# Kernel tuning notes

Measured on AMD Instinct MI355X. Metric: run time of the kernel, lower is better.

## Reference

```python
import jax, jax.numpy as jnp
import numpy as np

R = 4          # self.radius
NS = 256       # self.out_num_samples


def conv2d(x, w, b=None, padding=1, dilation=1):
    out = jax.lax.conv_general_dilated(
        x, w, window_strides=(1, 1),
        padding=[(padding, padding), (padding, padding)],
        rhs_dilation=(dilation, dilation),
        dimension_numbers=('NCHW', 'OIHW', 'NCHW'))
    if b is not None:
        out = out + b[None, :, None, None]
    return out


def depth_regression(logits):
    # softmax over 256 depth hypotheses, then expectation over a 9-wide
    # window centered at the argmax (clamped to [0, NS-1]).
    prob = jax.nn.softmax(logits, axis=1)                      # [B,256,H,W]
    amax = jnp.argmax(prob, axis=1, keepdims=True)             # [B,1,H,W] int
    offs = jnp.arange(-R, R + 1).reshape(1, 2 * R + 1, 1, 1)
    idx = jnp.clip(amax + offs, 0, NS - 1)                     # [B,9,H,W]
    p = jnp.take_along_axis(prob, idx, axis=1)                 # [B,9,H,W]
    num = jnp.sum(idx.astype(prob.dtype) * p, axis=1, keepdims=True)
    den = 1e-6 + jnp.sum(p, axis=1, keepdims=True)
    nd = (num / den) / (NS - 1.0)                              # [B,1,H,W]
    return nd, prob


def setup_inputs() -> dict:
    key = jax.random.key(0)
    ks = jax.random.split(key, 16)
    B, H, W = 4, 256, 320
    HD = 32            # hidden_dim
    CD = 32            # corr channels; input_dim = CD + 1 = 33
    CIN = HD + 1 + CD  # 65, GRU conv input channels

    def w(k, shape):
        fan = int(np.prod(shape[1:]))
        return (jax.random.normal(k, shape, jnp.float32) / np.sqrt(fan)).astype(jnp.float32)

    return {
        'hidden': jnp.tanh(jax.random.normal(ks[0], (B, HD, H, W), jnp.float32)),
        'normalized_depth': jax.random.uniform(ks[1], (B, 1, H, W), dtype=jnp.float32),
        'corr': jax.random.normal(ks[2], (B, CD, H, W), jnp.float32),
        # ConvGRU params (3x3, padding 1, with bias)
        'convz_w': w(ks[3], (HD, CIN, 3, 3)), 'convz_b': jnp.zeros((HD,), jnp.float32),
        'convr_w': w(ks[4], (HD, CIN, 3, 3)), 'convr_b': jnp.zeros((HD,), jnp.float32),
        'convq_w': w(ks[5], (HD, CIN, 3, 3)), 'convq_b': jnp.zeros((HD,), jnp.float32),
        # depth_head: 3x3 dil2 (no bias) -> 1x1 (no bias) -> 1x1 (bias)
        'dh1_w': w(ks[6], (32, HD, 3, 3)),
        'dh2_w': w(ks[7], (64, 32, 1, 1)),
        'dh3_w': w(ks[8], (NS, 64, 1, 1)), 'dh3_b': jnp.zeros((NS,), jnp.float32),
        # confidence_head: 3x3 dil2 (no bias) -> 1x1 (bias)
        'ch1_w': w(ks[9], (32, HD, 3, 3)),
        'ch2_w': w(ks[10], (1, 32, 1, 1)), 'ch2_b': jnp.zeros((1,), jnp.float32),
    }


def reference(hidden, normalized_depth, corr,
              convz_w, convz_b, convr_w, convr_b, convq_w, convq_b,
              dh1_w, dh2_w, dh3_w, dh3_b, ch1_w, ch2_w, ch2_b):
    # cat = [normalized_depth, corr]
    x = jnp.concatenate([normalized_depth, corr], axis=1)      # [B,33,H,W]
    # ConvGRU (confidence=None branch)
    hx = jnp.concatenate([hidden, x], axis=1)                  # [B,65,H,W]
    z = jax.nn.sigmoid(conv2d(hx, convz_w, convz_b))
    r = jax.nn.sigmoid(conv2d(hx, convr_w, convr_b))
    q = jnp.tanh(conv2d(jnp.concatenate([r * hidden, x], axis=1), convq_w, convq_b))
    h = (1.0 - z) * hidden + z * q                             # [B,32,H,W]
    # confidence head (confidence_flag=True)
    conf0 = conv2d(jax.nn.relu(conv2d(h, ch1_w, padding=2, dilation=2)),
                   ch2_w, ch2_b, padding=0)                    # [B,1,H,W]
    conf = jax.nn.sigmoid(conf0)
    # depth head
    t = jax.nn.relu(conv2d(h, dh1_w, padding=2, dilation=2))
    t = jax.nn.relu(conv2d(t, dh2_w, padding=0))
    logits = conv2d(t, dh3_w, dh3_b, padding=0)                # [B,256,H,W]
    nd, prob = depth_regression(logits)
    return h, nd, prob, conf, conf0
```

## Files before the change

### kernel.cpp

```cpp
#include <hip/hip_runtime.h>

#define WDT 320
#define HGT 256
#define HWSZ 81920
#define NPIX 327680

__device__ __forceinline__ float sigm(float x){ return 1.0f/(1.0f + __expf(-x)); }
__device__ __forceinline__ float tanh_(float x){
  float e = __expf(-2.0f*fabsf(x));
  float t = (1.0f - e)/(1.0f + e);
  return x < 0.0f ? -t : t;
}

__global__ __launch_bounds__(256) void k_wprep(
    const float* __restrict__ zw, const float* __restrict__ rw,
    const float* __restrict__ qw, const float* __restrict__ d1w,
    const float* __restrict__ c1w, const float* __restrict__ d2w,
    const float* __restrict__ d3w,
    float* __restrict__ W1, float* __restrict__ W2, float* __restrict__ W3,
    float* __restrict__ Wd2, float* __restrict__ Wd3)
{
  const int N1 = 9*65*64, N2 = 9*65*32, N3 = 9*32*64, N4 = 32*64, N5 = 64*256;
  int i = blockIdx.x*256 + threadIdx.x;
  if (i < N1){
    int tc = i >> 6, co = i & 63;
    int tap = tc / 65, cin = tc % 65;
    float v = (co < 32) ? zw[(size_t)(co*65 + cin)*9 + tap]
                        : rw[(size_t)((co-32)*65 + cin)*9 + tap];
    W1[i] = v;
  } else if (i < N1 + N2){
    int j = i - N1;
    int tc = j >> 5, co = j & 31;
    int tap = tc / 65, cin = tc % 65;
    W2[j] = qw[(size_t)(co*65 + cin)*9 + tap];
  } else if (i < N1 + N2 + N3){
    int j = i - (N1 + N2);
    int tc = j >> 6, co = j & 63;
    int tap = tc >> 5, cin = tc & 31;
    float v = (co < 32) ? d1w[(size_t)(co*32 + cin)*9 + tap]
                        : c1w[(size_t)((co-32)*32 + cin)*9 + tap];
    W3[j] = v;
  } else if (i < N1 + N2 + N3 + N4){
    int j = i - (N1 + N2 + N3);
    int cin = j >> 6, co = j & 63;
    Wd2[j] = d2w[co*32 + cin];
  } else if (i < N1 + N2 + N3 + N4 + N5){
    int j = i - (N1 + N2 + N3 + N4);
    int cin = j >> 8, co = j & 255;
    Wd3[j] = d3w[co*64 + cin];
  }
}


__global__ __launch_bounds__(256) void k_gru1(
    const float* __restrict__ hidden, const float* __restrict__ ndp,
    const float* __restrict__ corr, const float* __restrict__ W1,
    const float* __restrict__ zb, const float* __restrict__ rb,
    float* __restrict__ zpl, float* __restrict__ rhpl)
{
  int bid = blockIdx.x;
  int pb = (bid & 7)*160 + (bid >> 3);
  int p = pb*256 + threadIdx.x;
  int row = p / WDT;
  int x = p - row*WDT;
  int yimg = row & (HGT-1);
  int b = row >> 8;
  size_t hbase = (size_t)b*32*HWSZ + (size_t)(p - b*HWSZ);
  float acc[64];
  #pragma unroll
  for (int i=0;i<64;++i) acc[i]=0.f;
  #pragma unroll
  for (int ty=0; ty<3; ++ty){
    int dy = ty-1;
    if ((unsigned)(yimg+dy) >= (unsigned)HGT) continue;
    #pragma unroll
    for (int tx=0; tx<3; ++tx){
      int dx = tx-1;
      bool okx = (unsigned)(x+dx) < (unsigned)WDT;
      int off = dy*WDT + dx;
      const float* wt = W1 + (ty*3+tx)*65*64;
      #pragma unroll 1
      for (int c=0;c<32;++c){
        float v = okx ? hidden[hbase + (size_t)c*HWSZ + off] : 0.f;
        const float* w = wt + c*64;
        #pragma unroll
        for (int i=0;i<64;++i) acc[i] = fmaf(w[i], v, acc[i]);
      }
      {
        float v = okx ? ndp[p + off] : 0.f;
        const float* w = wt + 32*64;
        #pragma unroll
        for (int i=0;i<64;++i) acc[i] = fmaf(w[i], v, acc[i]);
      }
      #pragma unroll 1
      for (int c=0;c<32;++c){
        float v = okx ? corr[hbase + (size_t)c*HWSZ + off] : 0.f;
        const float* w = wt + (33+c)*64;
        #pragma unroll
        for (int i=0;i<64;++i) acc[i] = fmaf(w[i], v, acc[i]);
      }
    }
  }
  #pragma unroll
  for (int c=0;c<32;++c)
    zpl[(size_t)c*NPIX + p] = sigm(acc[c] + zb[c]);
  #pragma unroll
  for (int c=0;c<32;++c){
    float r = sigm(acc[32+c] + rb[c]);
    rhpl[(size_t)c*NPIX + p] = r * hidden[hbase + (size_t)c*HWSZ];
  }
}

__global__ __launch_bounds__(256) void k_gru2(
    const float* __restrict__ hidden, const float* __restrict__ ndp,
    const float* __restrict__ corr, const float* __restrict__ rhpl,
    const float* __restrict__ zpl, const float* __restrict__ W2,
    const float* __restrict__ qb, float* __restrict__ out_h)
{
  int bid = blockIdx.x;
  int pb = (bid & 7)*160 + (bid >> 3);
  int p = pb*256 + threadIdx.x;
  int row = p / WDT;
  int x = p - row*WDT;
  int yimg = row & (HGT-1);
  int b = row >> 8;
  size_t hbase = (size_t)b*32*HWSZ + (size_t)(p - b*HWSZ);
  float acc[32];
  #pragma unroll
  for (int i=0;i<32;++i) acc[i]=0.f;
  #pragma unroll
  for (int ty=0; ty<3; ++ty){
    int dy = ty-1;
    if ((unsigned)(yimg+dy) >= (unsigned)HGT) continue;
    #pragma unroll
    for (int tx=0; tx<3; ++tx){
      int dx = tx-1;
      bool okx = (unsigned)(x+dx) < (unsigned)WDT;
      int off = dy*WDT + dx;
      const float* wt = W2 + (ty*3+tx)*65*32;
      #pragma unroll 1
      for (int c=0;c<32;++c){
        float v = okx ? rhpl[(size_t)c*NPIX + p + off] : 0.f;
        const float* w = wt + c*32;
        #pragma unroll
        for (int i=0;i<32;++i) acc[i] = fmaf(w[i], v, acc[i]);
      }
      {
        float v = okx ? ndp[p + off] : 0.f;
        const float* w = wt + 32*32;
        #pragma unroll
        for (int i=0;i<32;++i) acc[i] = fmaf(w[i], v, acc[i]);
      }
      #pragma unroll 1
      for (int c=0;c<32;++c){
        float v = okx ? corr[hbase + (size_t)c*HWSZ + off] : 0.f;
        const float* w = wt + (33+c)*32;
        #pragma unroll
        for (int i=0;i<32;++i) acc[i] = fmaf(w[i], v, acc[i]);
      }
    }
  }
  #pragma unroll
  for (int c=0;c<32;++c){
    float qv = tanh_(acc[c] + qb[c]);
    float z  = zpl[(size_t)c*NPIX + p];
    float h0 = hidden[hbase + (size_t)c*HWSZ];
    out_h[hbase + (size_t)c*HWSZ] = (1.0f - z)*h0 + z*qv;
  }
}

__global__ __launch_bounds__(256) void k_heads(
    const float* __restrict__ out_h, const float* __restrict__ W3,
    const float* __restrict__ c2w, const float* __restrict__ c2b,
    float* __restrict__ t1pl, float* __restrict__ out_conf, float* __restrict__ out_conf0)
{
  int bid = blockIdx.x;
  int pb = (bid & 7)*160 + (bid >> 3);
  int p = pb*256 + threadIdx.x;
  int row = p / WDT;
  int x = p - row*WDT;
  int yimg = row & (HGT-1);
  int b = row >> 8;
  size_t hbase = (size_t)b*32*HWSZ + (size_t)(p - b*HWSZ);
  float acc[64];
  #pragma unroll
  for (int i=0;i<64;++i) acc[i]=0.f;
  #pragma unroll
  for (int ty=0; ty<3; ++ty){
    int dy = (ty-1)*2;
    if ((unsigned)(yimg+dy) >= (unsigned)HGT) continue;
    #pragma unroll
    for (int tx=0; tx<3; ++tx){
      int dx = (tx-1)*2;
      bool okx = (unsigned)(x+dx) < (unsigned)WDT;
      int off = dy*WDT + dx;
      const float* wt = W3 + (ty*3+tx)*32*64;
      #pragma unroll 1
      for (int c=0;c<32;++c){
        float v = okx ? out_h[hbase + (size_t)c*HWSZ + off] : 0.f;
        const float* w = wt + c*64;
        #pragma unroll
        for (int i=0;i<64;++i) acc[i] = fmaf(w[i], v, acc[i]);
      }
    }
  }
  #pragma unroll
  for (int c=0;c<32;++c)
    t1pl[(size_t)c*NPIX + p] = fmaxf(acc[c], 0.f);
  float conf0 = c2b[0];
  #pragma unroll
  for (int i=0;i<32;++i)
    conf0 = fmaf(fmaxf(acc[32+i], 0.f), c2w[i], conf0);
  out_conf0[p] = conf0;
  out_conf[p]  = sigm(conf0);
}

__global__ __launch_bounds__(256) void k_depth(
    const float* __restrict__ t1pl, const float* __restrict__ Wd2,
    const float* __restrict__ Wd3, const float* __restrict__ d3b,
    float* __restrict__ out_prob, float* __restrict__ out_nd)
{
  __shared__ float t2l[64][65];
  __shared__ float redA[4][64];
  __shared__ int   redI[4][64];
  __shared__ float redB[4][64];
  __shared__ float redC[4][64];
  int tid = threadIdx.x, lane = tid & 63;
  int wvu = __builtin_amdgcn_readfirstlane(tid >> 6);
  int p = blockIdx.x*64 + lane;
  float a1[16];
  #pragma unroll
  for (int i=0;i<16;++i) a1[i]=0.f;
  const float* Wd2b = Wd2 + wvu*16;
  #pragma unroll 2
  for (int c=0;c<32;++c){
    float v = t1pl[(size_t)c*NPIX + p];
    const float* w = Wd2b + c*64;
    #pragma unroll
    for (int i=0;i<16;++i) a1[i] = fmaf(w[i], v, a1[i]);
  }
  #pragma unroll
  for (int i=0;i<16;++i) t2l[lane][wvu*16+i] = fmaxf(a1[i], 0.f);
  __syncthreads();
  float acc[64];
  #pragma unroll
  for (int i=0;i<64;++i) acc[i]=0.f;
  const float* Wd3b = Wd3 + wvu*64;
  #pragma unroll 2
  for (int c=0;c<64;++c){
    float v = t2l[lane][c];
    const float* w = Wd3b + c*256;
    #pragma unroll
    for (int i=0;i<64;++i) acc[i] = fmaf(w[i], v, acc[i]);
  }
  const float* bb = d3b + wvu*64;
  float mx = -1e30f; int am = 0;
  #pragma unroll
  for (int i=0;i<64;++i){
    float l = acc[i] + bb[i];
    acc[i] = l;
    if (l > mx){ mx = l; am = wvu*64+i; }
  }
  redA[wvu][lane] = mx; redI[wvu][lane] = am;
  __syncthreads();
  float gmx = redA[0][lane]; int gam = redI[0][lane];
  #pragma unroll
  for (int w2=1; w2<4; ++w2){
    float m = redA[w2][lane]; int a = redI[w2][lane];
    if (m > gmx || (m == gmx && a < gam)){ gmx = m; gam = a; }
  }
  float s = 0.f;
  #pragma unroll
  for (int i=0;i<64;++i){
    float e = __expf(acc[i] - gmx);
    acc[i] = e; s += e;
  }
  redB[wvu][lane] = s;
  __syncthreads();
  float gs = redB[0][lane] + redB[1][lane] + redB[2][lane] + redB[3][lane];
  float inv = 1.0f / gs;
  int b = p / HWSZ;
  int qq = p - b*HWSZ;
  size_t obase = (size_t)b*256*HWSZ + qq;
  int lo = gam - 4, hi = gam + 4;
  float num = 0.f, den = 0.f;
  #pragma unroll
  for (int i=0;i<64;++i){
    int m = wvu*64 + i;
    float pr = acc[i] * inv;
    out_prob[obase + (size_t)m*HWSZ] = pr;
    int mlt = (m >= lo && m <= hi) ? 1 : 0;
    if (m == 0 && lo < 0) mlt = 1 - lo;
    if (m == 255 && hi > 255) mlt = hi - 254;
    num += (float)(m*mlt) * pr;
    den += (float)mlt * pr;
  }
  redA[wvu][lane] = num; redC[wvu][lane] = den;
  __syncthreads();
  if (wvu == 0){
    float tn = redA[0][lane]+redA[1][lane]+redA[2][lane]+redA[3][lane];
    float td = redC[0][lane]+redC[1][lane]+redC[2][lane]+redC[3][lane];
    out_nd[p] = (tn / (1e-6f + td)) * (1.0f/255.0f);
  }
}

extern "C" void kernel_launch(void* const* d_in, const int* in_sizes, int n_in,
                              void* d_out, int out_size, void* d_ws, size_t ws_size,
                              hipStream_t stream)
{
  const float* hidden = (const float*)d_in[0];
  const float* ndp    = (const float*)d_in[1];
  const float* corr   = (const float*)d_in[2];
  const float* zw  = (const float*)d_in[3];
  const float* zb  = (const float*)d_in[4];
  const float* rw  = (const float*)d_in[5];
  const float* rb  = (const float*)d_in[6];
  const float* qw  = (const float*)d_in[7];
  const float* qb  = (const float*)d_in[8];
  const float* d1w = (const float*)d_in[9];
  const float* d2w = (const float*)d_in[10];
  const float* d3w = (const float*)d_in[11];
  const float* d3b = (const float*)d_in[12];
  const float* c1w = (const float*)d_in[13];
  const float* c2w = (const float*)d_in[14];
  const float* c2b = (const float*)d_in[15];
  float* out = (float*)d_out;

  float* ws   = (float*)d_ws;
  float* zpl  = ws;
  float* rhpl = ws + 10485760;
  float* t1pl = ws + 20971520;
  float* W1   = ws + 31457280;
  float* W2   = W1 + 37440;
  float* W3   = W2 + 18720;
  float* Wd2  = W3 + 18432;
  float* Wd3  = Wd2 + 2048;

  float* out_h     = out;
  float* out_nd    = out + 10485760;
  float* out_prob  = out + 10813440;
  float* out_conf  = out + 94699520;
  float* out_conf0 = out + 95027200;

  k_wprep<<<364, 256, 0, stream>>>(zw, rw, qw, d1w, c1w, d2w, d3w, W1, W2, W3, Wd2, Wd3);
  k_gru1 <<<NPIX/256, 256, 0, stream>>>(hidden, ndp, corr, W1, zb, rb, zpl, rhpl);
  k_gru2 <<<NPIX/256, 256, 0, stream>>>(hidden, ndp, corr, rhpl, zpl, W2, qb, out_h);
  k_heads<<<NPIX/256, 256, 0, stream>>>(out_h, W3, c2w, c2b, t1pl, out_conf, out_conf0);
  k_depth<<<NPIX/64, 256, 0, stream>>>(t1pl, Wd2, Wd3, d3b, out_prob, out_nd);
}
```

Baseline: 1.251 ms.

## Reorder conv loops channel-outer with precomputed tap offsets and masks

Reorders the three direct-convolution kernels so the channel loop is outermost and the nine taps are fully unrolled inside it. Per-tap neighbour offsets and a 0/1 validity mask are computed once per thread, which removes branches from the inner loop. The batch index is made wave-uniform via readfirstlane. The weight-prep layout changes to channel-major to match, so each channel's 9x64 weights are contiguous scalar loads. The cost is extra registers for the offsets and masks, and a multiply by the mask that replaces the skipped border rows.

```diff
diff --git a/kernel.cpp b/kernel.cpp
--- a/kernel.cpp
+++ b/kernel.cpp
@@ -23,20 +23,20 @@
   const int N1 = 9*65*64, N2 = 9*65*32, N3 = 9*32*64, N4 = 32*64, N5 = 64*256;
   int i = blockIdx.x*256 + threadIdx.x;
   if (i < N1){
-    int tc = i >> 6, co = i & 63;
-    int tap = tc / 65, cin = tc % 65;
+    int cin = i / 576, r = i % 576;
+    int tap = r >> 6, co = r & 63;
     float v = (co < 32) ? zw[(size_t)(co*65 + cin)*9 + tap]
                         : rw[(size_t)((co-32)*65 + cin)*9 + tap];
     W1[i] = v;
   } else if (i < N1 + N2){
     int j = i - N1;
-    int tc = j >> 5, co = j & 31;
-    int tap = tc / 65, cin = tc % 65;
+    int cin = j / 288, r = j % 288;
+    int tap = r >> 5, co = r & 31;
     W2[j] = qw[(size_t)(co*65 + cin)*9 + tap];
   } else if (i < N1 + N2 + N3){
     int j = i - (N1 + N2);
-    int tc = j >> 6, co = j & 63;
-    int tap = tc >> 5, cin = tc & 31;
+    int cin = j / 576, r = j % 576;
+    int tap = r >> 6, co = r & 63;
     float v = (co < 32) ? d1w[(size_t)(co*32 + cin)*9 + tap]
                         : c1w[(size_t)((co-32)*32 + cin)*9 + tap];
     W3[j] = v;
@@ -64,41 +64,57 @@
   int row = p / WDT;
   int x = p - row*WDT;
   int yimg = row & (HGT-1);
-  int b = row >> 8;
-  size_t hbase = (size_t)b*32*HWSZ + (size_t)(p - b*HWSZ);
+  int b = __builtin_amdgcn_readfirstlane(row >> 8);
+  int q = p - b*HWSZ;
+  int vo[9]; float mf[9];
+  #pragma unroll
+  for (int ty=0; ty<3; ++ty){
+    #pragma unroll
+    for (int tx=0; tx<3; ++tx){
+      int dy = ty-1, dx = tx-1;
+      bool ok = ((unsigned)(yimg+dy) < (unsigned)HGT) && ((unsigned)(x+dx) < (unsigned)WDT);
+      vo[ty*3+tx] = ok ? (q + dy*WDT + dx) : q;
+      mf[ty*3+tx] = ok ? 1.0f : 0.0f;
+    }
+  }
+  const float* hb = hidden + (size_t)b*32*HWSZ;
+  const float* cb = corr   + (size_t)b*32*HWSZ;
+  const float* nb = ndp    + (size_t)b*HWSZ;
   float acc[64];
   #pragma unroll
   for (int i=0;i<64;++i) acc[i]=0.f;
-  #pragma unroll
-  for (int ty=0; ty<3; ++ty){
-    int dy = ty-1;
-    if ((unsigned)(yimg+dy) >= (unsigned)HGT) continue;
-    #pragma unroll
-    for (int tx=0; tx<3; ++tx){
-      int dx = tx-1;
-      bool okx = (unsigned)(x+dx) < (unsigned)WDT;
-      int off = dy*WDT + dx;
-      const float* wt = W1 + (ty*3+tx)*65*64;
-      #pragma unroll 1
-      for (int c=0;c<32;++c){
-        float v = okx ? hidden[hbase + (size_t)c*HWSZ + off] : 0.f;
-        const float* w = wt + c*64;
-        #pragma unroll
-        for (int i=0;i<64;++i) acc[i] = fmaf(w[i], v, acc[i]);
-      }
-      {
-        float v = okx ? ndp[p + off] : 0.f;
-        const float* w = wt + 32*64;
-        #pragma unroll
-        for (int i=0;i<64;++i) acc[i] = fmaf(w[i], v, acc[i]);
-      }
-      #pragma unroll 1
-      for (int c=0;c<32;++c){
-        float v = okx ? corr[hbase + (size_t)c*HWSZ + off] : 0.f;
-        const float* w = wt + (33+c)*64;
-        #pragma unroll
-        for (int i=0;i<64;++i) acc[i] = fmaf(w[i], v, acc[i]);
-      }
+  #pragma unroll 1
+  for (int c=0;c<32;++c){
+    const float* src = hb + (size_t)c*HWSZ;
+    const float* wr  = W1 + c*576;
+    #pragma unroll
+    for (int t=0;t<9;++t){
+      float vv = src[vo[t]] * mf[t];
+      const float* w = wr + t*64;
+      #pragma unroll
+      for (int i=0;i<64;++i) acc[i] = fmaf(w[i], vv, acc[i]);
+    }
+  }
+  {
+    const float* wr = W1 + 32*576;
+    #pragma unroll
+    for (int t=0;t<9;++t){
+      float vv = nb[vo[t]] * mf[t];
+      const float* w = wr + t*64;
+      #pragma unroll
+      for (int i=0;i<64;++i) acc[i] = fmaf(w[i], vv, acc[i]);
+    }
+  }
+  #pragma unroll 1
+  for (int c=0;c<32;++c){
+    const float* src = cb + (size_t)c*HWSZ;
+    const float* wr  = W1 + (33+c)*576;
+    #pragma unroll
+    for (int t=0;t<9;++t){
+      float vv = src[vo[t]] * mf[t];
+      const float* w = wr + t*64;
+      #pragma unroll
+      for (int i=0;i<64;++i) acc[i] = fmaf(w[i], vv, acc[i]);
     }
   }
   #pragma unroll
@@ -107,7 +123,7 @@
   #pragma unroll
   for (int c=0;c<32;++c){
     float r = sigm(acc[32+c] + rb[c]);
-    rhpl[(size_t)c*NPIX + p] = r * hidden[hbase + (size_t)c*HWSZ];
+    rhpl[(size_t)c*NPIX + p] = r * hb[q + (size_t)c*HWSZ];
   }
 }
 
@@ -123,49 +139,66 @@
   int row = p / WDT;
   int x = p - row*WDT;
   int yimg = row & (HGT-1);
-  int b = row >> 8;
-  size_t hbase = (size_t)b*32*HWSZ + (size_t)(p - b*HWSZ);
+  int b = __builtin_amdgcn_readfirstlane(row >> 8);
+  int q = p - b*HWSZ;
+  int vo[9]; float mf[9];
+  #pragma unroll
+  for (int ty=0; ty<3; ++ty){
+    #pragma unroll
+    for (int tx=0; tx<3; ++tx){
+      int dy = ty-1, dx = tx-1;
+      bool ok = ((unsigned)(yimg+dy) < (unsigned)HGT) && ((unsigned)(x+dx) < (unsigned)WDT);
+      vo[ty*3+tx] = ok ? (q + dy*WDT + dx) : q;
+      mf[ty*3+tx] = ok ? 1.0f : 0.0f;
+    }
+  }
+  const float* hb = hidden + (size_t)b*32*HWSZ;
+  const float* cb = corr   + (size_t)b*32*HWSZ;
+  const float* nb = ndp    + (size_t)b*HWSZ;
+  const float* rb_ = rhpl  + (size_t)b*HWSZ;
   float acc[32];
   #pragma unroll
   for (int i=0;i<32;++i) acc[i]=0.f;
-  #pragma unroll
-  for (int ty=0; ty<3; ++ty){
-    int dy = ty-1;
-    if ((unsigned)(yimg+dy) >= (unsigned)HGT) continue;
-    #pragma unroll
-    for (int tx=0; tx<3; ++tx){
-      int dx = tx-1;
-      bool okx = (unsigned)(x+dx) < (unsigned)WDT;
-      int off = dy*WDT + dx;
-      const float* wt = W2 + (ty*3+tx)*65*32;
-      #pragma unroll 1
-      for (int c=0;c<32;++c){
-        float v = okx ? rhpl[(size_t)c*NPIX + p + off] : 0.f;
-        const float* w = wt + c*32;
-        #pragma unroll
-        for (int i=0;i<32;++i) acc[i] = fmaf(w[i], v, acc[i]);
-      }
-      {
-        float v = okx ? ndp[p + off] : 0.f;
-        const float* w = wt + 32*32;
-        #pragma unroll
-        for (int i=0;i<32;++i) acc[i] = fmaf(w[i], v, acc[i]);
-      }
-      #pragma unroll 1
-      for (int c=0;c<32;++c){
-        float v = okx ? corr[hbase + (size_t)c*HWSZ + off] : 0.f;
-        const float* w = wt + (33+c)*32;
-        #pragma unroll
-        for (int i=0;i<32;++i) acc[i] = fmaf(w[i], v, acc[i]);
-      }
+  #pragma unroll 1
+  for (int c=0;c<32;++c){
+    const float* src = rb_ + (size_t)c*NPIX;
+    const float* wr  = W2 + c*288;
+    #pragma unroll
+    for (int t=0;t<9;++t){
+      float vv = src[vo[t]] * mf[t];
+      const float* w = wr + t*32;
+      #pragma unroll
+      for (int i=0;i<32;++i) acc[i] = fmaf(w[i], vv, acc[i]);
+    }
+  }
+  {
+    const float* wr = W2 + 32*288;
+    #pragma unroll
+    for (int t=0;t<9;++t){
+      float vv = nb[vo[t]] * mf[t];
+      const float* w = wr + t*32;
+      #pragma unroll
+      for (int i=0;i<32;++i) acc[i] = fmaf(w[i], vv, acc[i]);
+    }
+  }
+  #pragma unroll 1
+  for (int c=0;c<32;++c){
+    const float* src = cb + (size_t)c*HWSZ;
+    const float* wr  = W2 + (33+c)*288;
+    #pragma unroll
+    for (int t=0;t<9;++t){
+      float vv = src[vo[t]] * mf[t];
+      const float* w = wr + t*32;
+      #pragma unroll
+      for (int i=0;i<32;++i) acc[i] = fmaf(w[i], vv, acc[i]);
     }
   }
   #pragma unroll
   for (int c=0;c<32;++c){
     float qv = tanh_(acc[c] + qb[c]);
     float z  = zpl[(size_t)c*NPIX + p];
-    float h0 = hidden[hbase + (size_t)c*HWSZ];
-    out_h[hbase + (size_t)c*HWSZ] = (1.0f - z)*h0 + z*qv;
+    float h0 = hb[q + (size_t)c*HWSZ];
+    out_h[(size_t)b*32*HWSZ + (size_t)c*HWSZ + q] = (1.0f - z)*h0 + z*qv;
   }
 }
 
@@ -180,28 +213,33 @@
   int row = p / WDT;
   int x = p - row*WDT;
   int yimg = row & (HGT-1);
-  int b = row >> 8;
-  size_t hbase = (size_t)b*32*HWSZ + (size_t)(p - b*HWSZ);
+  int b = __builtin_amdgcn_readfirstlane(row >> 8);
+  int q = p - b*HWSZ;
+  int vo[9]; float mf[9];
+  #pragma unroll
+  for (int ty=0; ty<3; ++ty){
+    #pragma unroll
+    for (int tx=0; tx<3; ++tx){
+      int dy = (ty-1)*2, dx = (tx-1)*2;
+      bool ok = ((unsigned)(yimg+dy) < (unsigned)HGT) && ((unsigned)(x+dx) < (unsigned)WDT);
+      vo[ty*3+tx] = ok ? (q + dy*WDT + dx) : q;
+      mf[ty*3+tx] = ok ? 1.0f : 0.0f;
+    }
+  }
+  const float* hb = out_h + (size_t)b*32*HWSZ;
   float acc[64];
   #pragma unroll
   for (int i=0;i<64;++i) acc[i]=0.f;
-  #pragma unroll
-  for (int ty=0; ty<3; ++ty){
-    int dy = (ty-1)*2;
-    if ((unsigned)(yimg+dy) >= (unsigned)HGT) continue;
-    #pragma unroll
-    for (int tx=0; tx<3; ++tx){
-      int dx = (tx-1)*2;
-      bool okx = (unsigned)(x+dx) < (unsigned)WDT;
-      int off = dy*WDT + dx;
-      const float* wt = W3 + (ty*3+tx)*32*64;
-      #pragma unroll 1
-      for (int c=0;c<32;++c){
-        float v = okx ? out_h[hbase + (size_t)c*HWSZ + off] : 0.f;
-        const float* w = wt + c*64;
-        #pragma unroll
-        for (int i=0;i<64;++i) acc[i] = fmaf(w[i], v, acc[i]);
-      }
+  #pragma unroll 1
+  for (int c=0;c<32;++c){
+    const float* src = hb + (size_t)c*HWSZ;
+    const float* wr  = W3 + c*576;
+    #pragma unroll
+    for (int t=0;t<9;++t){
+      float vv = src[vo[t]] * mf[t];
+      const float* w = wr + t*64;
+      #pragma unroll
+      for (int i=0;i<64;++i) acc[i] = fmaf(w[i], vv, acc[i]);
     }
   }
   #pragma unroll
```

Result: no change. 1.261 ms (+0.8%).
